# Optimization experiments

Measured on AMD Instinct MI355X. Metric: run time of the kernel, lower is better.

The kernel has to match this reference:

```python
import jax, jax.numpy as jnp
import numpy as np
from jax import lax

SCORE_THRESHOLD = 0.01
NMS_THRESHOLD = 0.5
MAX_DETECTIONS = 100
PRE_NMS_TOPK = 512  # fixed-shape candidate pool per class (tf NMS is unbounded; 512 >> max_detections covers it)
NEG_INF = -jnp.inf


def setup_inputs() -> dict:
    key = jax.random.key(0)
    k1, k2, k3, k4, k5 = jax.random.split(key, 5)
    B, N, C = 32, 50000, 10
    # valid (x1,y1,x2,y2) boxes: random top-left + positive width/height
    xy = jax.random.uniform(k1, (B, N, 2), dtype=jnp.float32) * 500.0
    wh = jax.random.uniform(k2, (B, N, 2), dtype=jnp.float32) * 100.0 + 1.0
    boxes = jnp.concatenate([xy, xy + wh], axis=-1)
    classification = jax.random.uniform(k3, (B, N, C), dtype=jnp.float32)
    rotation = jax.random.normal(k4, (B, N, 3), dtype=jnp.float32)
    translation = jax.random.normal(k5, (B, N, 3), dtype=jnp.float32)
    return {"boxes": boxes, "classification": classification,
            "rotation": rotation, "translation": translation}


def _iou_matrix(b):  # b: (K,4) in (x1,y1,x2,y2)
    x1, y1, x2, y2 = b[:, 0], b[:, 1], b[:, 2], b[:, 3]
    area = (x2 - x1) * (y2 - y1)  # (K,)
    ix1 = jnp.maximum(x1[:, None], x1[None, :])
    iy1 = jnp.maximum(y1[:, None], y1[None, :])
    ix2 = jnp.minimum(x2[:, None], x2[None, :])
    iy2 = jnp.minimum(y2[:, None], y2[None, :])
    inter = jnp.maximum(ix2 - ix1, 0.0) * jnp.maximum(iy2 - iy1, 0.0)
    union = area[:, None] + area[None, :] - inter
    return jnp.where(union > 0.0, inter / union, 0.0)  # (K,K)


def _greedy_nms_keep(iou, valid):
    # iou: (K,K) for boxes already sorted by descending score; valid: (K,) bool
    K = iou.shape[0]
    def body(suppressed, xs):
        iou_row, valid_i, i = xs
        keep_i = valid_i & jnp.logical_not(suppressed[i])
        suppressed = jnp.where(keep_i, suppressed | (iou_row > NMS_THRESHOLD), suppressed)
        return suppressed, keep_i
    _, keep = lax.scan(body, jnp.zeros((K,), bool), (iou, valid, jnp.arange(K)))
    return keep


def _per_class(scores, boxes_i):
    # scores: (N,), boxes_i: (N,4) -> kept candidate scores (K,) (-inf where dropped) and anchor idx (K,)
    sc = jnp.where(scores > SCORE_THRESHOLD, scores, NEG_INF)
    vals, idx = lax.top_k(sc, PRE_NMS_TOPK)          # sorted desc
    valid = vals > SCORE_THRESHOLD                    # also false for -inf pads
    iou = _iou_matrix(boxes_i[idx])
    keep = _greedy_nms_keep(iou, valid)
    keep = keep & (jnp.cumsum(keep.astype(jnp.int32)) <= MAX_DETECTIONS)
    return jnp.where(keep, vals, NEG_INF), idx


def _per_image(boxes_i, cls_i, rot_i, trans_i):
    # boxes_i (N,4), cls_i (N,C), rot_i (N,3), trans_i (N,3)
    C = cls_i.shape[1]
    sc_ck, idx_ck = jax.vmap(_per_class, in_axes=(1, None))(cls_i, boxes_i)  # (C,K)
    labels_ck = jnp.broadcast_to(jnp.arange(C, dtype=jnp.int32)[:, None], sc_ck.shape)
    sc_flat = sc_ck.reshape(-1)
    idx_flat = idx_ck.reshape(-1)
    lab_flat = labels_ck.reshape(-1)
    top_scores, sel = lax.top_k(sc_flat, MAX_DETECTIONS)   # global top-k across classes
    sel_idx = idx_flat[sel]
    sel_lab = lab_flat[sel]
    valid = jnp.isfinite(top_scores)
    out_boxes = jnp.where(valid[:, None], boxes_i[sel_idx], -1.0)
    out_scores = jnp.where(valid, top_scores, -1.0)
    out_labels = jnp.where(valid, sel_lab, -1).astype(jnp.int32)
    out_rot = jnp.where(valid[:, None], rot_i[sel_idx], -1.0)
    out_trans = jnp.where(valid[:, None], trans_i[sel_idx], -1.0)
    return out_boxes, out_scores, out_labels, out_rot, out_trans


def reference(boxes, classification, rotation, translation):
    return jax.vmap(_per_image)(boxes, classification, rotation, translation)
```

## Files before the change

### kernel.cpp

```cpp
#include <hip/hip_runtime.h>
#include <math.h>

typedef unsigned int u32;
typedef unsigned long long u64;

constexpr int NB   = 32;
constexpr int NN   = 50000;
constexpr int NC   = 10;
constexpr int KK   = 512;
constexpr int MAXD = 100;
constexpr int CAP  = 2048;
constexpr int LCAP = 192;
constexpr int GCH  = 2500;
constexpr int KMAX = 1024;
constexpr u32 TBIN = 252;
constexpr int RLIM = 192;

constexpr int OFF_BOX = 0;
constexpr int OFF_SC  = NB * MAXD * 4;
constexpr int OFF_LB  = OFF_SC + NB * MAXD;
constexpr int OFF_RT  = OFF_LB + NB * MAXD;
constexpr int OFF_TR  = OFF_RT + NB * MAXD * 3;

__device__ __forceinline__ u32 ord_f32(float s) {
  u32 u = __float_as_uint(s);
  return (u & 0x80000000u) ? ~u : (u | 0x80000000u);
}
__device__ __forceinline__ float unord_f32(u32 o) {
  u32 u = (o & 0x80000000u) ? (o & 0x7FFFFFFFu) : ~o;
  return __uint_as_float(u);
}
__device__ __forceinline__ u64 make_key(float s, u32 i) {
  float sp = (s > 0.01f) ? s : -INFINITY;
  return ((u64)ord_f32(sp) << 32) | (u64)(u32)(~i);
}
__device__ __forceinline__ u32 digest16(float x) {
  if (!(x > 0.01f)) return 0;
  u32 q = (u32)(x * 65536.0f);
  return q > 65535u ? 65535u : q;
}
__device__ __forceinline__ float readlane_f(float v, int lane) {
  return __int_as_float(__builtin_amdgcn_readlane(__float_as_int(v), lane));
}
__device__ __forceinline__ u64 readlane_u64(u64 v, int lane) {
  u32 lo = __builtin_amdgcn_readlane((u32)v, lane);
  u32 hi = __builtin_amdgcn_readlane((u32)(v >> 32), lane);
  return ((u64)hi << 32) | lo;
}
__device__ __forceinline__ int clamp_idx(int idx) {
  return idx < 0 ? 0 : (idx >= NN ? NN - 1 : idx);
}

__global__ __launch_bounds__(512) void gather_kernel(
    const float* __restrict__ cls, u64* __restrict__ glist,
    u32* __restrict__ gcnt) {
  const int blk = blockIdx.x;
  const int b = blk / 20, ch = blk % 20;
  const float* src = cls + (size_t)b * NN * NC + (size_t)ch * GCH * NC;
  __shared__ u32 lcnt[NC];
  __shared__ u32 lbase[NC];
  __shared__ u64 lbuf[NC][LCAP];
  const int t = threadIdx.x;
  if (t < NC) lcnt[t] = 0;
  __syncthreads();
  for (int q = t; q < GCH * NC / 4; q += 512) {
    float4 v = ((const float4*)src)[q];
    float arr[4] = {v.x, v.y, v.z, v.w};
#pragma unroll
    for (int k = 0; k < 4; ++k) {
      int e = q * 4 + k;
      int c = e % 10;
      float x = arr[k];
      if ((digest16(x) >> 8) >= TBIN) {
        u32 idx = (u32)((ch * (GCH * NC) + e) / 10);
        u32 p = atomicAdd(&lcnt[c], 1u);
        if (p < (u32)LCAP) {
          lbuf[c][p] = make_key(x, idx);
        } else {
          u32 g = atomicAdd(&gcnt[b * NC + c], 1u);
          if (g < (u32)CAP) glist[(size_t)(b * NC + c) * CAP + g] = make_key(x, idx);
        }
      }
    }
  }
  __syncthreads();
  if (t < NC) {
    u32 n = min(lcnt[t], (u32)LCAP);
    lbase[t] = atomicAdd(&gcnt[b * NC + t], n);
  }
  __syncthreads();
  for (int c = 0; c < NC; ++c) {
    u32 n = min(lcnt[c], (u32)LCAP);
    u32 base = lbase[c];
    for (u32 i = t; i < n; i += 512) {
      u32 p = base + i;
      if (p < (u32)CAP) glist[(size_t)(b * NC + c) * CAP + p] = lbuf[c][i];
    }
  }
}

__global__ __launch_bounds__(512) void selnms_kernel(
    const float* __restrict__ cls, const u64* __restrict__ glist,
    const u32* __restrict__ gcnt, const float* __restrict__ boxes,
    int* __restrict__ tidx, float* __restrict__ ksc) {
  __shared__ __align__(16) unsigned char smem[38976];
  u64* cand = (u64*)smem;
  ushort (*prank)[8] = (ushort(*)[8])(smem + 8192);
  u64* sel = (u64*)(smem + 24576);
  float4* bx4 = (float4*)(smem + 28672);
  float* ars = (float*)(smem + 36864);
  u64* kmask = (u64*)(smem + 38912);
  u64 (*rowm)[8] = (u64(*)[8])smem;
  __shared__ int s_cnt, s_d;

  const int bc = (blockIdx.x & 7) * 40 + (blockIdx.x >> 3);
  const int b = bc / NC;
  const int t = threadIdx.x;
  const int lane = t & 63, wv = t >> 6;

  int M = (int)gcnt[bc];
  if (M >= KK && M <= KMAX) {
    for (int i = t; i < KMAX; i += 512)
      cand[i] = (i < M) ? glist[(size_t)bc * CAP + i] : (u64)i;
  } else {
    const int c = bc % NC;
    const float* sbase = cls + (size_t)b * NN * NC + c;
    u32* hist = (u32*)prank;
    for (int i = t; i < 4096; i += 512) hist[i] = 0;
    if (t == 0) s_cnt = 0;
    __syncthreads();
    for (int i = t; i < NN; i += 512)
      atomicAdd(&hist[digest16(sbase[(size_t)i * NC]) >> 4], 1u);
    __syncthreads();
    if (t == 0) {
      u32 run = 0, d = 1;
      for (int i = 4095; i >= 1; --i) {
        run += hist[i];
        if (run >= (u32)KK) { d = (u32)i; break; }
        d = 1;
      }
      s_d = (int)d;
    }
    __syncthreads();
    const u32 dstar = (u32)s_d;
    for (int i = t; i < KMAX; i += 512) cand[i] = (u64)i;
    __syncthreads();
    for (int i = t; i < NN; i += 512) {
      float x = sbase[(size_t)i * NC];
      u32 dg = digest16(x) >> 4;
      if (dg >= dstar && dg >= 1) {
        int p = atomicAdd(&s_cnt, 1);
        if (p < KMAX) cand[p] = make_key(x, (u32)i);
      }
    }
    __syncthreads();
    M = min(s_cnt, KMAX);
  }

  const u64 c0 = cand[t];
  const u64 c1 = cand[t + 512];
  const int pidx0 = clamp_idx((int)(~(u32)c0));
  const int pidx1 = clamp_idx((int)(~(u32)c1));
  const float4 pb0 = *(const float4*)(boxes + ((size_t)b * NN + pidx0) * 4);
  const float4 pb1 = *(const float4*)(boxes + ((size_t)b * NN + pidx1) * 4);

  sel[t] = make_key(-INFINITY, 0);
  __syncthreads();

  {
    u64 myk[16];
#pragma unroll
    for (int k = 0; k < 16; ++k) myk[k] = cand[lane + k * 64];
    int rnk[16];
#pragma unroll
    for (int k = 0; k < 16; ++k) rnk[k] = 0;
    const int j0 = wv * 128;
    const int rem = M - j0;
    const int jjmax = rem <= 0 ? 0 : (rem >= 128 ? 64 : ((rem + 1) >> 1));
    for (int jj = 0; jj < jjmax; ++jj) {
      const ulonglong2 v = *(const ulonglong2*)&cand[j0 + jj * 2];
#pragma unroll
      for (int k = 0; k < 16; ++k) {
        rnk[k] += (v.x > myk[k]) ? 1 : 0;
        rnk[k] += (v.y > myk[k]) ? 1 : 0;
      }
    }
#pragma unroll
    for (int k = 0; k < 16; ++k) prank[lane + k * 64][wv] = (ushort)rnk[k];
  }
  __syncthreads();
  {
    const uint4 pv0 = *(const uint4*)&prank[t][0];
    const int r0 = (int)(pv0.x & 0xFFFFu) + (int)(pv0.x >> 16) +
                   (int)(pv0.y & 0xFFFFu) + (int)(pv0.y >> 16) +
                   (int)(pv0.z & 0xFFFFu) + (int)(pv0.z >> 16) +
                   (int)(pv0.w & 0xFFFFu) + (int)(pv0.w >> 16);
    if (t < M && r0 < KK) {
      sel[r0] = c0;
      bx4[r0] = pb0;
      ars[r0] = (pb0.z - pb0.x) * (pb0.w - pb0.y);
    }
    const int i1 = t + 512;
    const uint4 pv1 = *(const uint4*)&prank[i1][0];
    const int r1 = (int)(pv1.x & 0xFFFFu) + (int)(pv1.x >> 16) +
                   (int)(pv1.y & 0xFFFFu) + (int)(pv1.y >> 16) +
                   (int)(pv1.z & 0xFFFFu) + (int)(pv1.z >> 16) +
                   (int)(pv1.w & 0xFFFFu) + (int)(pv1.w >> 16);
    if (i1 < M && r1 < KK) {
      sel[r1] = c1;
      bx4[r1] = pb1;
      ars[r1] = (pb1.z - pb1.x) * (pb1.w - pb1.y);
    }
  }
  __syncthreads();

  tidx[bc * KK + t] = clamp_idx((int)(~(u32)sel[t]));

  float jx1[8], jy1[8], jx2[8], jy2[8], jar[8];
#pragma unroll
  for (int q = 0; q < 8; ++q) {
    const float4 bb = bx4[q * 64 + lane];
    jx1[q] = bb.x; jy1[q] = bb.y; jx2[q] = bb.z; jy2[q] = bb.w;
    jar[q] = ars[q * 64 + lane];
  }
  __syncthreads();


#pragma unroll
  for (int g = 0; g < RLIM / 64; ++g) {
    for (int rr = 0; rr < 8; ++rr) {
      const int il = wv + 8 * rr;
      const int i = g * 64 + il;
      const float bix1 = readlane_f(jx1[g], il);
      const float biy1 = readlane_f(jy1[g], il);
      const float bix2 = readlane_f(jx2[g], il);
      const float biy2 = readlane_f(jy2[g], il);
      const float bia  = readlane_f(jar[g], il);
      u64 m[8];
#pragma unroll
      for (int q = 0; q < 8; ++q) {
        m[q] = 0;
        if (q >= g) {
          float ix1 = fmaxf(bix1, jx1[q]);
          float iy1 = fmaxf(biy1, jy1[q]);
          float ix2 = fminf(bix2, jx2[q]);
          float iy2 = fminf(biy2, jy2[q]);
          float iw = fmaxf(ix2 - ix1, 0.0f);
          float ih = fmaxf(iy2 - iy1, 0.0f);
          float inter = iw * ih;
          float uni = bia + jar[q] - inter;
          bool s = (uni > 0.0f) && ((inter - 0.5f * uni) > uni * 0x1p-25f);
          m[q] = __ballot(s);
        }
      }
      u64 word = m[0];
#pragma unroll
      for (int q = 1; q < 8; ++q) word = (lane == q) ? m[q] : word;
      if (lane < 8) rowm[i][lane] = word;
    }
  }
  __syncthreads();

  if (wv == 0) {
    u64 vw_[8], kw[8];
#pragma unroll
    for (int q = 0; q < 8; ++q) {
      const float sc = unord_f32((u32)(sel[q * 64 + lane] >> 32));
      vw_[q] = __ballot(sc > 0.01f);
      kw[q] = 0;
    }
    u64 vsup = 0;
    int count = 0;
    bool done = false;
#pragma unroll
    for (int w = 0; w < 8; ++w) {
      if (!done) {
        u64 av = vw_[w] & ~readlane_u64(vsup, w);
        while (av) {
          const int bbit = (int)__builtin_ctzll(av);
          const int i = w * 64 + bbit;
          kw[w] |= 1ull << bbit;
          if (++count == MAXD) { done = true; break; }
          if (w < RLIM / 64) {
            const u64 row = (lane < 8) ? rowm[i][lane] : 0;
            vsup |= row;
          } else {
            const float bix1 = readlane_f(jx1[w], bbit);
            const float biy1 = readlane_f(jy1[w], bbit);
            const float bix2 = readlane_f(jx2[w], bbit);
            const float biy2 = readlane_f(jy2[w], bbit);
            const float bia  = readlane_f(jar[w], bbit);
            u64 m[8];
#pragma unroll
            for (int q = 0; q < 8; ++q) {
              m[q] = 0;
              if (q >= w) {
                float ix1 = fmaxf(bix1, jx1[q]);
                float iy1 = fmaxf(biy1, jy1[q]);
                float ix2 = fminf(bix2, jx2[q]);
                float iy2 = fminf(biy2, jy2[q]);
                float iw = fmaxf(ix2 - ix1, 0.0f);
                float ih = fmaxf(iy2 - iy1, 0.0f);
                float inter = iw * ih;
                float uni = bia + jar[q] - inter;
                bool s = (uni > 0.0f) && ((inter - 0.5f * uni) > uni * 0x1p-25f);
                m[q] = __ballot(s);
              }
            }
            u64 word = m[0];
#pragma unroll
            for (int q = 1; q < 8; ++q) word = (lane == q) ? m[q] : word;
            vsup |= word;
          }
          const u64 mask_gt = (bbit == 63) ? 0ull : (~0ull << (bbit + 1));
          av = vw_[w] & ~readlane_u64(vsup, w) & mask_gt;
        }
      }
    }
    if (lane < 8) {
      u64 word = kw[0];
#pragma unroll
      for (int q = 1; q < 8; ++q) word = (lane == q) ? kw[q] : word;
      kmask[lane] = word;
    }
  }
  __syncthreads();
  {
    const float sc = unord_f32((u32)(sel[t] >> 32));
    const bool keep = (kmask[t >> 6] >> (t & 63)) & 1ull;
    ksc[(size_t)bc * KK + t] = keep ? sc : -INFINITY;
  }
}

__global__ __launch_bounds__(512) void final_kernel(
    const float* __restrict__ boxes, const float* __restrict__ rot,
    const float* __restrict__ trans, const int* __restrict__ tidx,
    const float* __restrict__ ksc, float* __restrict__ out) {
  const int b = blockIdx.x;
  __shared__ __align__(16) u64 ck[KMAX];
  __shared__ __align__(16) ushort prank[KMAX][8];
  __shared__ u64 top[MAXD];
  __shared__ int cnt;
  const int t = threadIdx.x;
  const int lane = t & 63, wv = t >> 6;
  if (t == 0) cnt = 0;
  if (t < MAXD) top[t] = make_key(-INFINITY, 0);
  for (int i = t; i < KMAX; i += 512) ck[i] = (u64)i;
  __syncthreads();
  for (int j = t; j < NC * KK; j += 512) {
    float s = ksc[b * NC * KK + j];
    if (s != -INFINITY) {
      int p = atomicAdd(&cnt, 1);
      if (p < KMAX) ck[p] = ((u64)ord_f32(s) << 32) | (u64)(u32)(~(u32)j);
    }
  }
  __syncthreads();
  const int n = min(cnt, KMAX);
  {
    u64 myk[16];
#pragma unroll
    for (int k = 0; k < 16; ++k) myk[k] = ck[lane + k * 64];
    int rnk[16];
#pragma unroll
    for (int k = 0; k < 16; ++k) rnk[k] = 0;
    const int j0 = wv * 128;
    const int rem = n - j0;
    const int jjmax = rem <= 0 ? 0 : (rem >= 128 ? 64 : ((rem + 1) >> 1));
    for (int jj = 0; jj < jjmax; ++jj) {
      const ulonglong2 v = *(const ulonglong2*)&ck[j0 + jj * 2];
#pragma unroll
      for (int k = 0; k < 16; ++k) {
        rnk[k] += (v.x > myk[k]) ? 1 : 0;
        rnk[k] += (v.y > myk[k]) ? 1 : 0;
      }
    }
#pragma unroll
    for (int k = 0; k < 16; ++k) prank[lane + k * 64][wv] = (ushort)rnk[k];
  }
  __syncthreads();
#pragma unroll
  for (int h = 0; h < 2; ++h) {
    const int i = h * 512 + t;
    const uint4 pv = *(const uint4*)&prank[i][0];
    const int r = (int)(pv.x & 0xFFFFu) + (int)(pv.x >> 16) +
                  (int)(pv.y & 0xFFFFu) + (int)(pv.y >> 16) +
                  (int)(pv.z & 0xFFFFu) + (int)(pv.z >> 16) +
                  (int)(pv.w & 0xFFFFu) + (int)(pv.w >> 16);
    if (i < n && r < MAXD) top[r] = ck[i];
  }
  __syncthreads();

  if (t < MAXD) {
    float b0 = -1.f, b1 = -1.f, b2 = -1.f, b3 = -1.f;
    float os = -1.f, ol = -1.f;
    float r0 = -1.f, r1 = -1.f, r2 = -1.f;
    float t0 = -1.f, t1 = -1.f, t2 = -1.f;
    const u64 k = top[t];
    const float sc = unord_f32((u32)(k >> 32));
    if (sc != -INFINITY) {
      int j = (int)(~(u32)k);
      int c = j >> 9, slot = j & (KK - 1);
      int idx = tidx[(b * NC + c) * KK + slot];
      os = sc;
      ol = (float)c;
      const float4 bx = *(const float4*)(boxes + ((size_t)b * NN + idx) * 4);
      b0 = bx.x; b1 = bx.y; b2 = bx.z; b3 = bx.w;
      const float* rp = rot + ((size_t)b * NN + idx) * 3;
      r0 = rp[0]; r1 = rp[1]; r2 = rp[2];
      const float* tp = trans + ((size_t)b * NN + idx) * 3;
      t0 = tp[0]; t1 = tp[1]; t2 = tp[2];
    }
    const int o = b * MAXD + t;
    out[OFF_BOX + (size_t)o * 4 + 0] = b0;
    out[OFF_BOX + (size_t)o * 4 + 1] = b1;
    out[OFF_BOX + (size_t)o * 4 + 2] = b2;
    out[OFF_BOX + (size_t)o * 4 + 3] = b3;
    out[OFF_SC + o] = os;
    out[OFF_LB + o] = ol;
    out[OFF_RT + (size_t)o * 3 + 0] = r0;
    out[OFF_RT + (size_t)o * 3 + 1] = r1;
    out[OFF_RT + (size_t)o * 3 + 2] = r2;
    out[OFF_TR + (size_t)o * 3 + 0] = t0;
    out[OFF_TR + (size_t)o * 3 + 1] = t1;
    out[OFF_TR + (size_t)o * 3 + 2] = t2;
  }
}

extern "C" void kernel_launch(void* const* d_in, const int* in_sizes, int n_in,
                              void* d_out, int out_size, void* d_ws, size_t ws_size,
                              hipStream_t stream) {
  const float* boxes = (const float*)d_in[0];
  const float* cls   = (const float*)d_in[1];
  const float* rot   = (const float*)d_in[2];
  const float* trans = (const float*)d_in[3];
  float* out = (float*)d_out;

  u64* glist = (u64*)d_ws;
  int* tidx  = (int*)(glist + (size_t)NB * NC * CAP);
  float* ksc = (float*)(tidx + NB * NC * KK);
  u32* gcnt  = (u32*)(ksc + NB * NC * KK);

  hipMemsetAsync(gcnt, 0, NB * NC * sizeof(u32), stream);
  gather_kernel<<<NB * 20, 512, 0, stream>>>(cls, glist, gcnt);
  selnms_kernel<<<NB * NC, 512, 0, stream>>>(cls, glist, gcnt, boxes, tidx, ksc);
  final_kernel<<<NB, 512, 0, stream>>>(boxes, rot, trans, tidx, ksc, out);
}
```

Measured before the change: 114.9 us.

## Resolve intra-word NMS suppression via register diagonal then batch row ORs

For the first precomputed-mask words, the serial greedy NMS loop now preloads each lane's diagonal 64-bit mask word into a register. Within-word suppression is resolved with readlane only, which takes the shared-memory load off the serial dependency chain. Cross-word suppression rows for the kept boxes are then ORed together afterward, two loads at a time. The row stride is padded from 8 to 9 u64 so the diagonal loads avoid LDS bank conflicts, at the cost of more shared memory for the mask region and a possible overlap with other buffers.

```diff
diff --git a/kernel.cpp b/kernel.cpp
--- a/kernel.cpp
+++ b/kernel.cpp
@@ -110,7 +110,7 @@
   float4* bx4 = (float4*)(smem + 28672);
   float* ars = (float*)(smem + 36864);
   u64* kmask = (u64*)(smem + 38912);
-  u64 (*rowm)[8] = (u64(*)[8])smem;
+  u64 (*rowm)[9] = (u64(*)[9])smem;
   __shared__ int s_cnt, s_d;
 
   const int bc = (blockIdx.x & 7) * 40 + (blockIdx.x >> 3);
@@ -269,22 +269,49 @@
       vw_[q] = __ballot(sc > 0.01f);
       kw[q] = 0;
     }
+    const u64 diag0 = rowm[0 * 64 + lane][0];
+    const u64 diag1 = rowm[1 * 64 + lane][1];
+    const u64 diag2 = rowm[2 * 64 + lane][2];
     u64 vsup = 0;
     int count = 0;
     bool done = false;
 #pragma unroll
     for (int w = 0; w < 8; ++w) {
       if (!done) {
-        u64 av = vw_[w] & ~readlane_u64(vsup, w);
-        while (av) {
-          const int bbit = (int)__builtin_ctzll(av);
-          const int i = w * 64 + bbit;
-          kw[w] |= 1ull << bbit;
-          if (++count == MAXD) { done = true; break; }
-          if (w < RLIM / 64) {
-            const u64 row = (lane < 8) ? rowm[i][lane] : 0;
-            vsup |= row;
-          } else {
+        u64 avail = vw_[w] & ~readlane_u64(vsup, w);
+        if (w < RLIM / 64) {
+          const u64 dg = (w == 0) ? diag0 : (w == 1) ? diag1 : diag2;
+          u64 kwm = 0;
+          while (avail) {
+            const int bbit = (int)__builtin_ctzll(avail);
+            kwm |= 1ull << bbit;
+            if (++count == MAXD) { done = true; break; }
+            const u64 rowd = readlane_u64(dg, bbit);
+            const u64 mask_gt = (bbit == 63) ? 0ull : (~0ull << (bbit + 1));
+            avail &= ~rowd & mask_gt;
+          }
+          kw[w] = kwm;
+          if (!done) {
+            u64 acc = 0, km = kwm;
+            while (km) {
+              const int b2 = (int)__builtin_ctzll(km);
+              km &= km - 1;
+              const u64 v1 = (lane < 8) ? rowm[w * 64 + b2][lane] : 0;
+              if (km) {
+                const int b3 = (int)__builtin_ctzll(km);
+                km &= km - 1;
+                const u64 v2 = (lane < 8) ? rowm[w * 64 + b3][lane] : 0;
+                acc |= v2;
+              }
+              acc |= v1;
+            }
+            vsup |= acc;
+          }
+        } else {
+          while (avail) {
+            const int bbit = (int)__builtin_ctzll(avail);
+            kw[w] |= 1ull << bbit;
+            if (++count == MAXD) { done = true; break; }
             const float bix1 = readlane_f(jx1[w], bbit);
             const float biy1 = readlane_f(jy1[w], bbit);
             const float bix2 = readlane_f(jx2[w], bbit);
@@ -311,9 +338,9 @@
 #pragma unroll
             for (int q = 1; q < 8; ++q) word = (lane == q) ? m[q] : word;
             vsup |= word;
+            const u64 mask_gt = (bbit == 63) ? 0ull : (~0ull << (bbit + 1));
+            avail = vw_[w] & ~readlane_u64(vsup, w) & mask_gt;
           }
-          const u64 mask_gt = (bbit == 63) ? 0ull : (~0ull << (bbit + 1));
-          av = vw_[w] & ~readlane_u64(vsup, w) & mask_gt;
         }
       }
     }
```

Result: no change. 115.0 us (+0.1%).
